# Kernel tuning notes

Hardware: AMD Instinct MI355X
Metric: run time of the kernel (lower is better)

Reference implementation:

```python
import jax, jax.numpy as jnp
import numpy as np
import math

B, S, H, NH = 2, 2048, 2048, 16
HD = H // NH
BASE = 10000.0


def _rope_tables():
    inv_freq = 1.0 / (BASE ** (np.arange(0, HD, 2, dtype=np.float32) / HD))
    t = np.arange(S, dtype=np.float32)
    freqs = np.einsum('i,j->ij', t, inv_freq)          # [S, HD/2]
    emb = np.concatenate([freqs, freqs], axis=-1)       # [S, HD]
    return jnp.asarray(np.cos(emb)), jnp.asarray(np.sin(emb))


def setup_inputs() -> dict:
    key = jax.random.key(0)
    ks = jax.random.split(key, 6)
    scale = 1.0 / math.sqrt(H)
    cos, sin = _rope_tables()
    causal = np.triu(np.full((S, S), -1e9, dtype=np.float32), k=1)
    attn_bias = jnp.broadcast_to(jnp.asarray(causal)[None, None], (B, 1, S, S))
    return {
        'hidden_states': jax.random.normal(ks[0], (B, S, H), jnp.float32),
        'masks': jnp.zeros((B, S, S), jnp.float32),
        'attn_bias': attn_bias,
        'cos': cos,
        'sin': sin,
        'wq': jax.random.normal(ks[1], (H, H), jnp.float32) * scale,
        'wk': jax.random.normal(ks[2], (H, H), jnp.float32) * scale,
        'wv': jax.random.normal(ks[3], (H, H), jnp.float32) * scale,
        'wo': jax.random.normal(ks[4], (H, H), jnp.float32) * scale,
        'position_ids': jnp.broadcast_to(jnp.arange(S, dtype=jnp.int64)[None], (B, S)),
    }


def _rotate_half(x):
    x1, x2 = x[..., : x.shape[-1] // 2], x[..., x.shape[-1] // 2:]
    return jnp.concatenate([-x2, x1], axis=-1)


def reference(hidden_states, masks, attn_bias, cos, sin, wq, wk, wv, wo, position_ids):
    b, s, h = hidden_states.shape
    nh, hd = NH, HD
    # QKV projections (torch Linear: x @ W.T), split heads -> [b, nh, s, hd]
    def proj(w):
        return (hidden_states @ w.T).reshape(b, s, nh, hd).transpose(0, 2, 1, 3)
    q, k, v = proj(wq), proj(wk), proj(wv)
    # RoPE
    cos_p = cos[position_ids][:, None]  # [b, 1, s, hd]
    sin_p = sin[position_ids][:, None]
    q = q * cos_p + _rotate_half(q) * sin_p
    k = k * cos_p + _rotate_half(k) * sin_p
    # attention scores with additive masks (mx_attn branch, fp math)
    att = jnp.einsum('bhqd,bhkd->bhqk', q / math.sqrt(hd), k)
    att = att + attn_bias + masks[:, None]
    att = jax.nn.softmax(att, axis=-1)
    out = jnp.einsum('bhqk,bhkd->bhqd', att, v)
    out = out.transpose(0, 2, 1, 3).reshape(b, s, h)
    return out @ wo.T
```

## Files before the change

kernel.cpp:

```cpp
#include <hip/hip_runtime.h>
#include <stdint.h>

#define B_  2
#define S_  2048
#define H_  2048
#define NH_ 16
#define HD_ 128

typedef __bf16 v8bf __attribute__((ext_vector_type(8)));
typedef float  v4f  __attribute__((ext_vector_type(4)));

__device__ __forceinline__ float b2f(unsigned short u) {
  union { unsigned int i; float f; } x; x.i = ((unsigned int)u) << 16; return x.f;
}
__device__ __forceinline__ unsigned short f2b(float f) {
  union { float f; unsigned int i; } x; x.f = f;
  unsigned int r = x.i + 0x7FFFu + ((x.i >> 16) & 1u);
  return (unsigned short)(r >> 16);
}

__device__ __forceinline__ void async16(const void* g, void* l) {
  __builtin_amdgcn_global_load_lds(
      (const __attribute__((address_space(1))) void*)g,
      (__attribute__((address_space(3))) void*)l, 16, 0, 0);
}

__global__ __launch_bounds__(256) void cvt_f32_bf16(const float* __restrict__ src,
                                                    unsigned short* __restrict__ dst,
                                                    int n4) {
  int i = blockIdx.x * 256 + threadIdx.x;
  if (i < n4) {
    float4 f = *(const float4*)(src + (size_t)i * 4);
    ushort4 u;
    u.x = f2b(f.x); u.y = f2b(f.y); u.z = f2b(f.z); u.w = f2b(f.w);
    *(ushort4*)(dst + (size_t)i * 4) = u;
  }
}

__device__ __forceinline__ void gemm_tile_nt(const unsigned short* __restrict__ A,
                                             const unsigned short* __restrict__ Bm,
                                             int m0, int n0, int Kdim,
                                             unsigned short* As, unsigned short* Bs,
                                             v4f (&acc)[4][4]) {
  const int tid = threadIdx.x;
  const int lane = tid & 63, w = tid >> 6;
  const int lr = lane & 15, lg = lane >> 4;
  const int wm = (w >> 1) * 64, wn = (w & 1) * 64;

  for (int k0 = 0; k0 < Kdim; k0 += 32) {
    __syncthreads();
#pragma unroll
    for (int i = 0; i < 2; ++i) {
      const int cbase = i * 256 + w * 64;
      const int cc = cbase + lane;
      const int row = cc >> 2, col = (cc & 3) << 3;
      async16(A  + (size_t)(m0 + row) * Kdim + k0 + col, (char*)As + (size_t)cbase * 16);
      async16(Bm + (size_t)(n0 + row) * Kdim + k0 + col, (char*)Bs + (size_t)cbase * 16);
    }
    __syncthreads();
    v8bf a[4], bb[4];
#pragma unroll
    for (int i = 0; i < 4; i++) a[i]  = *(const v8bf*)(As + (wm + i * 16 + lr) * 32 + lg * 8);
#pragma unroll
    for (int i = 0; i < 4; i++) bb[i] = *(const v8bf*)(Bs + (wn + i * 16 + lr) * 32 + lg * 8);
#pragma unroll
    for (int mi = 0; mi < 4; mi++)
#pragma unroll
      for (int ni = 0; ni < 4; ni++)
        acc[mi][ni] = __builtin_amdgcn_mfma_f32_16x16x32_bf16(a[mi], bb[ni], acc[mi][ni], 0, 0, 0);
  }
}

__global__ __launch_bounds__(256, 2) void gemm_qkv(const unsigned short* __restrict__ X,
                                                   const unsigned short* __restrict__ Wq,
                                                   const unsigned short* __restrict__ Wk,
                                                   const unsigned short* __restrict__ Wv,
                                                   unsigned short* __restrict__ Qo,
                                                   unsigned short* __restrict__ Ko,
                                                   unsigned short* __restrict__ Vo) {
  __shared__ unsigned short As[128 * 32], Bs[128 * 32];
  const int m0 = blockIdx.x * 128;
  const int ny = blockIdx.y;
  const int sel = ny >> 4;
  const unsigned short* Bm = (sel == 0) ? Wq : (sel == 1 ? Wk : Wv);
  unsigned short* Out = (sel == 0) ? Qo : (sel == 1 ? Ko : Vo);
  const int n0 = (ny & 15) * 128;

  v4f acc[4][4];
#pragma unroll
  for (int i = 0; i < 4; i++)
#pragma unroll
    for (int j = 0; j < 4; j++) { v4f z = {0.f, 0.f, 0.f, 0.f}; acc[i][j] = z; }

  gemm_tile_nt(X, Bm, m0, n0, H_, As, Bs, acc);

  const int lane = threadIdx.x & 63, w = threadIdx.x >> 6;
  const int lr = lane & 15, lg = lane >> 4;
  const int wm = (w >> 1) * 64, wn = (w & 1) * 64;
#pragma unroll
  for (int mi = 0; mi < 4; mi++)
#pragma unroll
    for (int ni = 0; ni < 4; ni++)
#pragma unroll
      for (int r = 0; r < 4; r++)
        Out[(size_t)(m0 + wm + mi * 16 + lg * 4 + r) * H_ + n0 + wn + ni * 16 + lr] =
            f2b(acc[mi][ni][r]);
}

__global__ __launch_bounds__(256, 2) void gemm_out(const unsigned short* __restrict__ A,
                                                   const unsigned short* __restrict__ Wo,
                                                   float* __restrict__ Out) {
  __shared__ unsigned short As[128 * 32], Bs[128 * 32];
  const int m0 = blockIdx.x * 128;
  const int n0 = blockIdx.y * 128;

  v4f acc[4][4];
#pragma unroll
  for (int i = 0; i < 4; i++)
#pragma unroll
    for (int j = 0; j < 4; j++) { v4f z = {0.f, 0.f, 0.f, 0.f}; acc[i][j] = z; }

  gemm_tile_nt(A, Wo, m0, n0, H_, As, Bs, acc);

  const int lane = threadIdx.x & 63, w = threadIdx.x >> 6;
  const int lr = lane & 15, lg = lane >> 4;
  const int wm = (w >> 1) * 64, wn = (w & 1) * 64;
#pragma unroll
  for (int mi = 0; mi < 4; mi++)
#pragma unroll
    for (int ni = 0; ni < 4; ni++)
#pragma unroll
      for (int r = 0; r < 4; r++)
        Out[(size_t)(m0 + wm + mi * 16 + lg * 4 + r) * H_ + n0 + wn + ni * 16 + lr] =
            acc[mi][ni][r];
}

__global__ __launch_bounds__(256) void rope_kernel(unsigned short* __restrict__ Q,
                                                   unsigned short* __restrict__ K,
                                                   const float* __restrict__ cosT,
                                                   const float* __restrict__ sinT) {
  unsigned idx = blockIdx.x * 256 + threadIdx.x;
  int dq = (idx & 15) * 4;
  int h  = (idx >> 4) & 15;
  int s  = (idx >> 8) & 2047;
  int b  = idx >> 19;
  size_t base = ((size_t)(b * S_ + s)) * H_ + h * HD_;
  const float* cr = cosT + (size_t)s * HD_;
  const float* sr = sinT + (size_t)s * HD_;
  float c1[4], c2[4], s1[4], s2[4];
#pragma unroll
  for (int j = 0; j < 4; j++) {
    c1[j] = cr[dq + j]; c2[j] = cr[64 + dq + j];
    s1[j] = sr[dq + j]; s2[j] = sr[64 + dq + j];
  }
#pragma unroll
  for (int a = 0; a < 2; a++) {
    unsigned short* P = a == 0 ? Q : K;
    const float sc = (a == 0) ? 0.088388347648318447f : 1.0f;
    ushort4 u1 = *(ushort4*)(P + base + dq);
    ushort4 u2 = *(ushort4*)(P + base + 64 + dq);
    float x1[4] = {b2f(u1.x), b2f(u1.y), b2f(u1.z), b2f(u1.w)};
    float x2[4] = {b2f(u2.x), b2f(u2.y), b2f(u2.z), b2f(u2.w)};
    ushort4 o1, o2;
    o1.x = f2b((x1[0] * c1[0] - x2[0] * s1[0]) * sc);
    o1.y = f2b((x1[1] * c1[1] - x2[1] * s1[1]) * sc);
    o1.z = f2b((x1[2] * c1[2] - x2[2] * s1[2]) * sc);
    o1.w = f2b((x1[3] * c1[3] - x2[3] * s1[3]) * sc);
    o2.x = f2b((x2[0] * c2[0] + x1[0] * s2[0]) * sc);
    o2.y = f2b((x2[1] * c2[1] + x1[1] * s2[1]) * sc);
    o2.z = f2b((x2[2] * c2[2] + x1[2] * s2[2]) * sc);
    o2.w = f2b((x2[3] * c2[3] + x1[3] * s2[3]) * sc);
    *(ushort4*)(P + base + dq) = o1;
    *(ushort4*)(P + base + 64 + dq) = o2;
  }
}

__global__ __launch_bounds__(256) void transpose_v(const unsigned short* __restrict__ Vb,
                                                   unsigned short* __restrict__ Vt) {
  __shared__ unsigned short tile[64][130];
  const int tid = threadIdx.x;
  const int s0 = blockIdx.x * 64;
  const int h = blockIdx.y, b = blockIdx.z;
  for (int i = tid; i < 64 * 64; i += 256) {
    int s = i >> 6, dp = i & 63;
    *(ushort2*)&tile[s][dp * 2] =
        *(const ushort2*)(Vb + (size_t)(b * S_ + s0 + s) * H_ + h * HD_ + dp * 2);
  }
  __syncthreads();
  for (int i = tid; i < 128 * 64; i += 256) {
    int d = i >> 6, s = i & 63;
    Vt[((size_t)((b * NH_ + h) * HD_) + d) * S_ + s0 + s] = tile[s][d];
  }
}

#define KT_ 64

__global__ __launch_bounds__(256, 2) void attn_kernel(const unsigned short* __restrict__ Qb,
                                                      const unsigned short* __restrict__ Kb,
                                                      const unsigned short* __restrict__ Vt,
                                                      unsigned short* __restrict__ Ob) {
  __shared__ __align__(16) char smem[54272];
  unsigned short* Ks = (unsigned short*)smem;
  unsigned short* Vs = (unsigned short*)(smem + 17408);
  unsigned short* Ps = (unsigned short*)(smem + 35840);

  const int tid = threadIdx.x, lane = tid & 63, w = tid >> 6;
  const int lr = lane & 15, lg = lane >> 4;
  const int qt = blockIdx.x, h = blockIdx.y, b = blockIdx.z;
  const int q0 = qt * 128;
  const int wrow = q0 + w * 32;

  v8bf qf[2][4];
#pragma unroll
  for (int mt = 0; mt < 2; mt++)
#pragma unroll
    for (int ks = 0; ks < 4; ks++)
      qf[mt][ks] = *(const v8bf*)(Qb + (size_t)(b * S_ + wrow + mt * 16 + lr) * H_ +
                                  h * HD_ + ks * 32 + lg * 8);

  v4f o[2][8];
#pragma unroll
  for (int mt = 0; mt < 2; mt++)
#pragma unroll
    for (int nt = 0; nt < 8; nt++) { v4f z = {0.f, 0.f, 0.f, 0.f}; o[mt][nt] = z; }
  float mst[2][4], lst[2][4];
#pragma unroll
  for (int mt = 0; mt < 2; mt++)
#pragma unroll
    for (int r = 0; r < 4; r++) { mst[mt][r] = -1e30f; lst[mt][r] = 0.f; }

  const int nkt = (q0 + 128) / KT_;
  for (int kt = 0; kt < nkt; kt++) {
    const int k0 = kt * KT_;
    __syncthreads();
    for (int i = 0; i < 5; ++i) {
      int cbase = i * 256 + w * 64;
      if (cbase < 1088) {
        int cc = cbase + lane;
        int row = cc / 17, pos = cc % 17;
        int p2 = (pos == 16) ? 0 : pos;
        async16(Kb + (size_t)(b * S_ + k0 + row) * H_ + h * HD_ + p2 * 8,
                (char*)Ks + (size_t)cbase * 16);
      }
    }
    for (int i = 0; i < 5; ++i) {
      int cbase = i * 256 + w * 64;
      if (cbase < 1152) {
        int cc = cbase + lane;
        int row = cc / 9, pos = cc % 9;
        int p2 = (pos == 8) ? 0 : pos;
        async16(Vt + ((size_t)((b * NH_ + h) * HD_ + row)) * S_ + k0 + p2 * 8,
                (char*)Vs + (size_t)cbase * 16);
      }
    }
    __syncthreads();

    if (k0 <= wrow + 31) {
      v4f sacc[2][4];
#pragma unroll
      for (int mt = 0; mt < 2; mt++)
#pragma unroll
        for (int nt = 0; nt < 4; nt++) { v4f z = {0.f, 0.f, 0.f, 0.f}; sacc[mt][nt] = z; }
#pragma unroll
      for (int nt = 0; nt < 4; nt++) {
        v8bf kf[4];
#pragma unroll
        for (int ks = 0; ks < 4; ks++)
          kf[ks] = *(const v8bf*)(Ks + (nt * 16 + lr) * 136 + ks * 32 + lg * 8);
#pragma unroll
        for (int mt = 0; mt < 2; mt++)
#pragma unroll
          for (int ks = 0; ks < 4; ks++)
            sacc[mt][nt] =
                __builtin_amdgcn_mfma_f32_16x16x32_bf16(qf[mt][ks], kf[ks], sacc[mt][nt], 0, 0, 0);
      }
      if (k0 + KT_ - 1 > wrow) {
#pragma unroll
        for (int mt = 0; mt < 2; mt++)
#pragma unroll
          for (int nt = 0; nt < 4; nt++)
#pragma unroll
            for (int r = 0; r < 4; r++) {
              int key = k0 + nt * 16 + lr;
              int query = wrow + mt * 16 + lg * 4 + r;
              if (key > query) sacc[mt][nt][r] = -1e30f;
            }
      }
#pragma unroll
      for (int mt = 0; mt < 2; mt++) {
        float rmax[4], alpha[4], rsum[4];
#pragma unroll
        for (int r = 0; r < 4; r++) {
          float v = fmaxf(fmaxf(sacc[mt][0][r], sacc[mt][1][r]),
                          fmaxf(sacc[mt][2][r], sacc[mt][3][r]));
#pragma unroll
          for (int off = 8; off >= 1; off >>= 1) v = fmaxf(v, __shfl_xor(v, off, 64));
          rmax[r] = v;
        }
#pragma unroll
        for (int r = 0; r < 4; r++) {
          float mnew = fmaxf(mst[mt][r], rmax[r]);
          alpha[r] = __expf(mst[mt][r] - mnew);
          mst[mt][r] = mnew;
          rsum[r] = 0.f;
        }
#pragma unroll
        for (int nt = 0; nt < 4; nt++)
#pragma unroll
          for (int r = 0; r < 4; r++) {
            float p = __expf(sacc[mt][nt][r] - mst[mt][r]);
            rsum[r] += p;
            Ps[w * 2304 + (mt * 16 + lg * 4 + r) * 72 + nt * 16 + lr] = f2b(p);
          }
#pragma unroll
        for (int r = 0; r < 4; r++) {
#pragma unroll
          for (int off = 8; off >= 1; off >>= 1) rsum[r] += __shfl_xor(rsum[r], off, 64);
          lst[mt][r] = lst[mt][r] * alpha[r] + rsum[r];
        }
#pragma unroll
        for (int nt = 0; nt < 8; nt++)
#pragma unroll
          for (int r = 0; r < 4; r++) o[mt][nt][r] *= alpha[r];
      }
      asm volatile("" ::: "memory");
      v8bf af[2][2];
#pragma unroll
      for (int mt = 0; mt < 2; mt++)
#pragma unroll
        for (int ks = 0; ks < 2; ks++)
          af[mt][ks] = *(const v8bf*)(Ps + w * 2304 + (mt * 16 + lr) * 72 + ks * 32 + lg * 8);
#pragma unroll
      for (int nt = 0; nt < 8; nt++) {
        v8bf bv[2];
#pragma unroll
        for (int ks = 0; ks < 2; ks++)
          bv[ks] = *(const v8bf*)(Vs + (nt * 16 + lr) * 72 + ks * 32 + lg * 8);
#pragma unroll
        for (int mt = 0; mt < 2; mt++)
#pragma unroll
          for (int ks = 0; ks < 2; ks++)
            o[mt][nt] = __builtin_amdgcn_mfma_f32_16x16x32_bf16(af[mt][ks], bv[ks], o[mt][nt], 0, 0, 0);
      }
    }
  }
#pragma unroll
  for (int mt = 0; mt < 2; mt++) {
    float inv[4];
#pragma unroll
    for (int r = 0; r < 4; r++) inv[r] = 1.f / lst[mt][r];
#pragma unroll
    for (int nt = 0; nt < 8; nt++)
#pragma unroll
      for (int r = 0; r < 4; r++) {
        int row = wrow + mt * 16 + lg * 4 + r;
        int col = h * HD_ + nt * 16 + lr;
        Ob[(size_t)(b * S_ + row) * H_ + col] = f2b(o[mt][nt][r] * inv[r]);
      }
  }
}

extern "C" void kernel_launch(void* const* d_in, const int* in_sizes, int n_in,
                              void* d_out, int out_size, void* d_ws, size_t ws_size,
                              hipStream_t stream) {
  const float* hidden = (const float*)d_in[0];
  const float* cosT = (const float*)d_in[3];
  const float* sinT = (const float*)d_in[4];
  const float* wq = (const float*)d_in[5];
  const float* wk = (const float*)d_in[6];
  const float* wv = (const float*)d_in[7];
  const float* wo = (const float*)d_in[8];
  float* out = (float*)d_out;

  char* p = (char*)d_ws;
  const size_t SZ_X = (size_t)4096 * 2048 * 2;
  const size_t SZ_W = (size_t)2048 * 2048 * 2;
  unsigned short* Xb  = (unsigned short*)p; p += SZ_X;
  unsigned short* Wqb = (unsigned short*)p; p += SZ_W;
  unsigned short* Wkb = (unsigned short*)p; p += SZ_W;
  unsigned short* Wvb = (unsigned short*)p; p += SZ_W;
  unsigned short* Wob = (unsigned short*)p; p += SZ_W;
  unsigned short* Qb  = (unsigned short*)p; p += SZ_X;
  unsigned short* Kb  = (unsigned short*)p; p += SZ_X;
  unsigned short* Vb  = (unsigned short*)p; p += SZ_X;
  unsigned short* Vt  = (unsigned short*)p; p += SZ_X;
  unsigned short* Ob  = Vb;

  cvt_f32_bf16<<<8192, 256, 0, stream>>>(hidden, Xb, 2097152);
  cvt_f32_bf16<<<4096, 256, 0, stream>>>(wq, Wqb, 1048576);
  cvt_f32_bf16<<<4096, 256, 0, stream>>>(wk, Wkb, 1048576);
  cvt_f32_bf16<<<4096, 256, 0, stream>>>(wv, Wvb, 1048576);
  cvt_f32_bf16<<<4096, 256, 0, stream>>>(wo, Wob, 1048576);

  gemm_qkv<<<dim3(32, 48), 256, 0, stream>>>(Xb, Wqb, Wkb, Wvb, Qb, Kb, Vb);
  rope_kernel<<<4096, 256, 0, stream>>>(Qb, Kb, cosT, sinT);
  transpose_v<<<dim3(32, 16, 2), 256, 0, stream>>>(Vb, Vt);
  attn_kernel<<<dim3(16, 16, 2), 256, 0, stream>>>(Qb, Kb, Vt, Ob);
  gemm_out<<<dim3(32, 16), 256, 0, stream>>>(Ob, Wob, out);
}
```

Before: 490.7 us.

## Fuse RoPE and V transpose into QKV GEMM, balance causal attention blocks

Merges the five conversion launches into one kernel. Folds RoPE and the Q scaling (with log2e so exp2f can be used) and the V transpose into the QKV GEMM epilogue, which removes the separate rope and transpose passes over global memory. Reshapes the GEMM warp tiling to 32x128 per warp so each warp holds both RoPE halves of a head. The attention kernel now pairs causal query tiles qp and 15-qp in one 512-thread block to balance work, truncates P to bf16 instead of rounding it, and stages P per m-tile to shrink LDS use. The truncation and the strided epilogue stores of Vt and cos/sin may cost some accuracy or bandwidth.

```diff
diff --git a/kernel.cpp b/kernel.cpp
--- a/kernel.cpp
+++ b/kernel.cpp
@@ -25,27 +25,41 @@
       (__attribute__((address_space(3))) void*)l, 16, 0, 0);
 }
 
-__global__ __launch_bounds__(256) void cvt_f32_bf16(const float* __restrict__ src,
-                                                    unsigned short* __restrict__ dst,
-                                                    int n4) {
-  int i = blockIdx.x * 256 + threadIdx.x;
-  if (i < n4) {
-    float4 f = *(const float4*)(src + (size_t)i * 4);
-    ushort4 u;
-    u.x = f2b(f.x); u.y = f2b(f.y); u.z = f2b(f.z); u.w = f2b(f.w);
-    *(ushort4*)(dst + (size_t)i * 4) = u;
-  }
+__global__ __launch_bounds__(256) void cvt_all(const float* __restrict__ hid,
+                                               const float* __restrict__ wq,
+                                               const float* __restrict__ wk,
+                                               const float* __restrict__ wv,
+                                               const float* __restrict__ wo,
+                                               unsigned short* __restrict__ Xb,
+                                               unsigned short* __restrict__ Wqb,
+                                               unsigned short* __restrict__ Wkb,
+                                               unsigned short* __restrict__ Wvb,
+                                               unsigned short* __restrict__ Wob) {
+  int bid = blockIdx.x;
+  const float* src;
+  unsigned short* dst;
+  int rel;
+  if (bid < 8192)       { src = hid; dst = Xb;  rel = bid; }
+  else if (bid < 12288) { src = wq;  dst = Wqb; rel = bid - 8192; }
+  else if (bid < 16384) { src = wk;  dst = Wkb; rel = bid - 12288; }
+  else if (bid < 20480) { src = wv;  dst = Wvb; rel = bid - 16384; }
+  else                  { src = wo;  dst = Wob; rel = bid - 20480; }
+  int i = rel * 256 + threadIdx.x;
+  float4 f = *(const float4*)(src + (size_t)i * 4);
+  ushort4 u;
+  u.x = f2b(f.x); u.y = f2b(f.y); u.z = f2b(f.z); u.w = f2b(f.w);
+  *(ushort4*)(dst + (size_t)i * 4) = u;
 }
 
 __device__ __forceinline__ void gemm_tile_nt(const unsigned short* __restrict__ A,
                                              const unsigned short* __restrict__ Bm,
                                              int m0, int n0, int Kdim,
                                              unsigned short* As, unsigned short* Bs,
-                                             v4f (&acc)[4][4]) {
+                                             v4f (&acc)[2][8]) {
   const int tid = threadIdx.x;
   const int lane = tid & 63, w = tid >> 6;
   const int lr = lane & 15, lg = lane >> 4;
-  const int wm = (w >> 1) * 64, wn = (w & 1) * 64;
+  const int wm = w * 32;
 
   for (int k0 = 0; k0 < Kdim; k0 += 32) {
     __syncthreads();
@@ -58,15 +72,15 @@
       async16(Bm + (size_t)(n0 + row) * Kdim + k0 + col, (char*)Bs + (size_t)cbase * 16);
     }
     __syncthreads();
-    v8bf a[4], bb[4];
-#pragma unroll
-    for (int i = 0; i < 4; i++) a[i]  = *(const v8bf*)(As + (wm + i * 16 + lr) * 32 + lg * 8);
-#pragma unroll
-    for (int i = 0; i < 4; i++) bb[i] = *(const v8bf*)(Bs + (wn + i * 16 + lr) * 32 + lg * 8);
-#pragma unroll
-    for (int mi = 0; mi < 4; mi++)
-#pragma unroll
-      for (int ni = 0; ni < 4; ni++)
+    v8bf a[2], bb[8];
+#pragma unroll
+    for (int i = 0; i < 2; i++) a[i]  = *(const v8bf*)(As + (wm + i * 16 + lr) * 32 + lg * 8);
+#pragma unroll
+    for (int i = 0; i < 8; i++) bb[i] = *(const v8bf*)(Bs + (i * 16 + lr) * 32 + lg * 8);
+#pragma unroll
+    for (int mi = 0; mi < 2; mi++)
+#pragma unroll
+      for (int ni = 0; ni < 8; ni++)
         acc[mi][ni] = __builtin_amdgcn_mfma_f32_16x16x32_bf16(a[mi], bb[ni], acc[mi][ni], 0, 0, 0);
   }
 }
@@ -75,36 +89,63 @@
                                                    const unsigned short* __restrict__ Wq,
                                                    const unsigned short* __restrict__ Wk,
                                                    const unsigned short* __restrict__ Wv,
+                                                   const float* __restrict__ cosT,
+                                                   const float* __restrict__ sinT,
                                                    unsigned short* __restrict__ Qo,
                                                    unsigned short* __restrict__ Ko,
-                                                   unsigned short* __restrict__ Vo) {
+                                                   unsigned short* __restrict__ Vt) {
   __shared__ unsigned short As[128 * 32], Bs[128 * 32];
   const int m0 = blockIdx.x * 128;
   const int ny = blockIdx.y;
   const int sel = ny >> 4;
+  const int h = ny & 15;
   const unsigned short* Bm = (sel == 0) ? Wq : (sel == 1 ? Wk : Wv);
-  unsigned short* Out = (sel == 0) ? Qo : (sel == 1 ? Ko : Vo);
-  const int n0 = (ny & 15) * 128;
-
-  v4f acc[4][4];
-#pragma unroll
-  for (int i = 0; i < 4; i++)
-#pragma unroll
-    for (int j = 0; j < 4; j++) { v4f z = {0.f, 0.f, 0.f, 0.f}; acc[i][j] = z; }
+  const int n0 = h * 128;
+
+  v4f acc[2][8];
+#pragma unroll
+  for (int i = 0; i < 2; i++)
+#pragma unroll
+    for (int j = 0; j < 8; j++) { v4f z = {0.f, 0.f, 0.f, 0.f}; acc[i][j] = z; }
 
   gemm_tile_nt(X, Bm, m0, n0, H_, As, Bs, acc);
 
   const int lane = threadIdx.x & 63, w = threadIdx.x >> 6;
   const int lr = lane & 15, lg = lane >> 4;
-  const int wm = (w >> 1) * 64, wn = (w & 1) * 64;
-#pragma unroll
-  for (int mi = 0; mi < 4; mi++)
-#pragma unroll
-    for (int ni = 0; ni < 4; ni++)
-#pragma unroll
-      for (int r = 0; r < 4; r++)
-        Out[(size_t)(m0 + wm + mi * 16 + lg * 4 + r) * H_ + n0 + wn + ni * 16 + lr] =
-            f2b(acc[mi][ni][r]);
+  const int rbase = m0 + w * 32;
+
+  if (sel < 2) {
+    unsigned short* Out = (sel == 0) ? Qo : Ko;
+    const float sc = (sel == 0) ? (float)(0.08838834764831845 * 1.4426950408889634) : 1.0f;
+#pragma unroll
+    for (int mi = 0; mi < 2; mi++)
+#pragma unroll
+      for (int ni = 0; ni < 4; ni++)
+#pragma unroll
+        for (int r = 0; r < 4; r++) {
+          int row = rbase + mi * 16 + lg * 4 + r;
+          int s = row & 2047;
+          int d = ni * 16 + lr;
+          float c  = cosT[(size_t)s * HD_ + d];
+          float sn = sinT[(size_t)s * HD_ + d];
+          float x1 = acc[mi][ni][r], x2 = acc[mi][ni + 4][r];
+          Out[(size_t)row * H_ + n0 + d]      = f2b((x1 * c - x2 * sn) * sc);
+          Out[(size_t)row * H_ + n0 + d + 64] = f2b((x2 * c + x1 * sn) * sc);
+        }
+  } else {
+#pragma unroll
+    for (int mi = 0; mi < 2; mi++)
+#pragma unroll
+      for (int ni = 0; ni < 8; ni++) {
+        int row0 = rbase + mi * 16 + lg * 4;
+        int b = row0 >> 11, s0 = row0 & 2047;
+        int d = ni * 16 + lr;
+        ushort4 u;
+        u.x = f2b(acc[mi][ni][0]); u.y = f2b(acc[mi][ni][1]);
+        u.z = f2b(acc[mi][ni][2]); u.w = f2b(acc[mi][ni][3]);
+        *(ushort4*)(Vt + ((size_t)((b * NH_ + h) * HD_) + d) * S_ + s0) = u;
+      }
+  }
 }
 
 __global__ __launch_bounds__(256, 2) void gemm_out(const unsigned short* __restrict__ A,
@@ -114,88 +155,29 @@
   const int m0 = blockIdx.x * 128;
   const int n0 = blockIdx.y * 128;
 
-  v4f acc[4][4];
-#pragma unroll
-  for (int i = 0; i < 4; i++)
-#pragma unroll
-    for (int j = 0; j < 4; j++) { v4f z = {0.f, 0.f, 0.f, 0.f}; acc[i][j] = z; }
+  v4f acc[2][8];
+#pragma unroll
+  for (int i = 0; i < 2; i++)
+#pragma unroll
+    for (int j = 0; j < 8; j++) { v4f z = {0.f, 0.f, 0.f, 0.f}; acc[i][j] = z; }
 
   gemm_tile_nt(A, Wo, m0, n0, H_, As, Bs, acc);
 
   const int lane = threadIdx.x & 63, w = threadIdx.x >> 6;
   const int lr = lane & 15, lg = lane >> 4;
-  const int wm = (w >> 1) * 64, wn = (w & 1) * 64;
-#pragma unroll
-  for (int mi = 0; mi < 4; mi++)
-#pragma unroll
-    for (int ni = 0; ni < 4; ni++)
+#pragma unroll
+  for (int mi = 0; mi < 2; mi++)
+#pragma unroll
+    for (int ni = 0; ni < 8; ni++)
 #pragma unroll
       for (int r = 0; r < 4; r++)
-        Out[(size_t)(m0 + wm + mi * 16 + lg * 4 + r) * H_ + n0 + wn + ni * 16 + lr] =
+        Out[(size_t)(m0 + w * 32 + mi * 16 + lg * 4 + r) * H_ + n0 + ni * 16 + lr] =
             acc[mi][ni][r];
 }
 
-__global__ __launch_bounds__(256) void rope_kernel(unsigned short* __restrict__ Q,
-                                                   unsigned short* __restrict__ K,
-                                                   const float* __restrict__ cosT,
-                                                   const float* __restrict__ sinT) {
-  unsigned idx = blockIdx.x * 256 + threadIdx.x;
-  int dq = (idx & 15) * 4;
-  int h  = (idx >> 4) & 15;
-  int s  = (idx >> 8) & 2047;
-  int b  = idx >> 19;
-  size_t base = ((size_t)(b * S_ + s)) * H_ + h * HD_;
-  const float* cr = cosT + (size_t)s * HD_;
-  const float* sr = sinT + (size_t)s * HD_;
-  float c1[4], c2[4], s1[4], s2[4];
-#pragma unroll
-  for (int j = 0; j < 4; j++) {
-    c1[j] = cr[dq + j]; c2[j] = cr[64 + dq + j];
-    s1[j] = sr[dq + j]; s2[j] = sr[64 + dq + j];
-  }
-#pragma unroll
-  for (int a = 0; a < 2; a++) {
-    unsigned short* P = a == 0 ? Q : K;
-    const float sc = (a == 0) ? 0.088388347648318447f : 1.0f;
-    ushort4 u1 = *(ushort4*)(P + base + dq);
-    ushort4 u2 = *(ushort4*)(P + base + 64 + dq);
-    float x1[4] = {b2f(u1.x), b2f(u1.y), b2f(u1.z), b2f(u1.w)};
-    float x2[4] = {b2f(u2.x), b2f(u2.y), b2f(u2.z), b2f(u2.w)};
-    ushort4 o1, o2;
-    o1.x = f2b((x1[0] * c1[0] - x2[0] * s1[0]) * sc);
-    o1.y = f2b((x1[1] * c1[1] - x2[1] * s1[1]) * sc);
-    o1.z = f2b((x1[2] * c1[2] - x2[2] * s1[2]) * sc);
-    o1.w = f2b((x1[3] * c1[3] - x2[3] * s1[3]) * sc);
-    o2.x = f2b((x2[0] * c2[0] + x1[0] * s2[0]) * sc);
-    o2.y = f2b((x2[1] * c2[1] + x1[1] * s2[1]) * sc);
-    o2.z = f2b((x2[2] * c2[2] + x1[2] * s2[2]) * sc);
-    o2.w = f2b((x2[3] * c2[3] + x1[3] * s2[3]) * sc);
-    *(ushort4*)(P + base + dq) = o1;
-    *(ushort4*)(P + base + 64 + dq) = o2;
-  }
-}
-
-__global__ __launch_bounds__(256) void transpose_v(const unsigned short* __restrict__ Vb,
-                                                   unsigned short* __restrict__ Vt) {
-  __shared__ unsigned short tile[64][130];
-  const int tid = threadIdx.x;
-  const int s0 = blockIdx.x * 64;
-  const int h = blockIdx.y, b = blockIdx.z;
-  for (int i = tid; i < 64 * 64; i += 256) {
-    int s = i >> 6, dp = i & 63;
-    *(ushort2*)&tile[s][dp * 2] =
-        *(const ushort2*)(Vb + (size_t)(b * S_ + s0 + s) * H_ + h * HD_ + dp * 2);
-  }
-  __syncthreads();
-  for (int i = tid; i < 128 * 64; i += 256) {
-    int d = i >> 6, s = i & 63;
-    Vt[((size_t)((b * NH_ + h) * HD_) + d) * S_ + s0 + s] = tile[s][d];
-  }
-}
-
 #define KT_ 64
 
-__global__ __launch_bounds__(256, 2) void attn_kernel(const unsigned short* __restrict__ Qb,
+__global__ __launch_bounds__(512, 2) void attn_kernel(const unsigned short* __restrict__ Qb,
                                                       const unsigned short* __restrict__ Kb,
                                                       const unsigned short* __restrict__ Vt,
                                                       unsigned short* __restrict__ Ob) {
@@ -206,9 +188,11 @@
 
   const int tid = threadIdx.x, lane = tid & 63, w = tid >> 6;
   const int lr = lane & 15, lg = lane >> 4;
-  const int qt = blockIdx.x, h = blockIdx.y, b = blockIdx.z;
-  const int q0 = qt * 128;
-  const int wrow = q0 + w * 32;
+  const int qp = blockIdx.x, h = blockIdx.y, b = blockIdx.z;
+
+  const int wtile = (w < 4) ? qp : (15 - qp);
+  const int wrow = wtile * 128 + (w & 3) * 32;
+  const int nkt = (16 - qp) * 2;
 
   v8bf qf[2][4];
 #pragma unroll
@@ -229,12 +213,12 @@
 #pragma unroll
     for (int r = 0; r < 4; r++) { mst[mt][r] = -1e30f; lst[mt][r] = 0.f; }
 
-  const int nkt = (q0 + 128) / KT_;
   for (int kt = 0; kt < nkt; kt++) {
     const int k0 = kt * KT_;
     __syncthreads();
-    for (int i = 0; i < 5; ++i) {
-      int cbase = i * 256 + w * 64;
+#pragma unroll
+    for (int i = 0; i < 3; ++i) {
+      int cbase = i * 512 + w * 64;
       if (cbase < 1088) {
         int cc = cbase + lane;
         int row = cc / 17, pos = cc % 17;
@@ -243,8 +227,9 @@
                 (char*)Ks + (size_t)cbase * 16);
       }
     }
-    for (int i = 0; i < 5; ++i) {
-      int cbase = i * 256 + w * 64;
+#pragma unroll
+    for (int i = 0; i < 3; ++i) {
+      int cbase = i * 512 + w * 64;
       if (cbase < 1152) {
         int cc = cbase + lane;
         int row = cc / 9, pos = cc % 9;
@@ -300,7 +285,7 @@
 #pragma unroll
         for (int r = 0; r < 4; r++) {
           float mnew = fmaxf(mst[mt][r], rmax[r]);
-          alpha[r] = __expf(mst[mt][r] - mnew);
+          alpha[r] = exp2f(mst[mt][r] - mnew);
           mst[mt][r] = mnew;
           rsum[r] = 0.f;
         }
@@ -308,9 +293,9 @@
         for (int nt = 0; nt < 4; nt++)
 #pragma unroll
           for (int r = 0; r < 4; r++) {
-            float p = __expf(sacc[mt][nt][r] - mst[mt][r]);
+            float p = exp2f(sacc[mt][nt][r] - mst[mt][r]);
+            sacc[mt][nt][r] = p;
             rsum[r] += p;
-            Ps[w * 2304 + (mt * 16 + lg * 4 + r) * 72 + nt * 16 + lr] = f2b(p);
           }
 #pragma unroll
         for (int r = 0; r < 4; r++) {
@@ -323,24 +308,33 @@
 #pragma unroll
           for (int r = 0; r < 4; r++) o[mt][nt][r] *= alpha[r];
       }
-      asm volatile("" ::: "memory");
-      v8bf af[2][2];
-#pragma unroll
-      for (int mt = 0; mt < 2; mt++)
+      v8bf bv[8][2];
+#pragma unroll
+      for (int nt = 0; nt < 8; nt++)
 #pragma unroll
         for (int ks = 0; ks < 2; ks++)
-          af[mt][ks] = *(const v8bf*)(Ps + w * 2304 + (mt * 16 + lr) * 72 + ks * 32 + lg * 8);
-#pragma unroll
-      for (int nt = 0; nt < 8; nt++) {
-        v8bf bv[2];
+          bv[nt][ks] = *(const v8bf*)(Vs + (nt * 16 + lr) * 72 + ks * 32 + lg * 8);
+#pragma unroll
+      for (int mt = 0; mt < 2; mt++) {
+#pragma unroll
+        for (int nt = 0; nt < 4; nt++)
+#pragma unroll
+          for (int r = 0; r < 4; r++) {
+            union { float f; unsigned u; } pu; pu.f = sacc[mt][nt][r];
+            Ps[w * 1152 + (lg * 4 + r) * 72 + nt * 16 + lr] =
+                (unsigned short)(pu.u >> 16);
+          }
+        asm volatile("" ::: "memory");
+        v8bf af[2];
 #pragma unroll
         for (int ks = 0; ks < 2; ks++)
-          bv[ks] = *(const v8bf*)(Vs + (nt * 16 + lr) * 72 + ks * 32 + lg * 8);
-#pragma unroll
-        for (int mt = 0; mt < 2; mt++)
+          af[ks] = *(const v8bf*)(Ps + w * 1152 + lr * 72 + ks * 32 + lg * 8);
+#pragma unroll
+        for (int nt = 0; nt < 8; nt++)
 #pragma unroll
           for (int ks = 0; ks < 2; ks++)
-            o[mt][nt] = __builtin_amdgcn_mfma_f32_16x16x32_bf16(af[mt][ks], bv[ks], o[mt][nt], 0, 0, 0);
+            o[mt][nt] = __builtin_amdgcn_mfma_f32_16x16x32_bf16(af[ks], bv[nt][ks], o[mt][nt], 0, 0, 0);
+        asm volatile("" ::: "memory");
       }
     }
   }
@@ -382,19 +376,11 @@
   unsigned short* Wob = (unsigned short*)p; p += SZ_W;
   unsigned short* Qb  = (unsigned short*)p; p += SZ_X;
   unsigned short* Kb  = (unsigned short*)p; p += SZ_X;
-  unsigned short* Vb  = (unsigned short*)p; p += SZ_X;
   unsigned short* Vt  = (unsigned short*)p; p += SZ_X;
-  unsigned short* Ob  = Vb;
-
-  cvt_f32_bf16<<<8192, 256, 0, stream>>>(hidden, Xb, 2097152);
-  cvt_f32_bf16<<<4096, 256, 0, stream>>>(wq, Wqb, 1048576);
-  cvt_f32_bf16<<<4096, 256, 0, stream>>>(wk, Wkb, 1048576);
-  cvt_f32_bf16<<<4096, 256, 0, stream>>>(wv, Wvb, 1048576);
-  cvt_f32_bf16<<<4096, 256, 0, stream>>>(wo, Wob, 1048576);
-
-  gemm_qkv<<<dim3(32, 48), 256, 0, stream>>>(Xb, Wqb, Wkb, Wvb, Qb, Kb, Vb);
-  rope_kernel<<<4096, 256, 0, stream>>>(Qb, Kb, cosT, sinT);
-  transpose_v<<<dim3(32, 16, 2), 256, 0, stream>>>(Vb, Vt);
-  attn_kernel<<<dim3(16, 16, 2), 256, 0, stream>>>(Qb, Kb, Vt, Ob);
+  unsigned short* Ob  = (unsigned short*)p; p += SZ_X;
+
+  cvt_all<<<24576, 256, 0, stream>>>(hidden, wq, wk, wv, wo, Xb, Wqb, Wkb, Wvb, Wob);
+  gemm_qkv<<<dim3(32, 48), 256, 0, stream>>>(Xb, Wqb, Wkb, Wvb, cosT, sinT, Qb, Kb, Vt);
+  attn_kernel<<<dim3(8, 16, 2), 512, 0, stream>>>(Qb, Kb, Vt, Ob);
   gemm_out<<<dim3(32, 16), 256, 0, stream>>>(Ob, Wob, out);
 }
```

New measurement: 458.0 us. 1.07x faster.
